# Performance work log

Measured on AMD Instinct MI355X. Metric: run time of the kernel, lower is better.

## Reference

```python
import jax, jax.numpy as jnp
import numpy as np

KERNEL_SIZE = 32
STRIDE = 16
NEG_INF = -1e30


def setup_inputs() -> dict:
    key = jax.random.key(0)
    ks = jax.random.split(key, 5)
    B, N, QH, KH, D = 1, 8192, 32, 2, 128
    q = jax.random.normal(ks[0], (B, N, QH, D), jnp.float32)
    k = jax.random.normal(ks[1], (B, N, KH, D), jnp.float32)
    v = jax.random.normal(ks[2], (B, N, KH, D), jnp.float32)
    weight = jax.random.uniform(ks[3], (KERNEL_SIZE,), jnp.float32)
    pe = jax.random.normal(ks[4], (KERNEL_SIZE, D), jnp.float32) * 0.02
    return {"q": q, "k": k, "v": v, "weight": weight, "pe": pe}


def block_compress(x, weight, pe, stride, kernel_size):
    # x: [B,N,H,D], weight: [K], pe: [K,D] -> y: [B,M,H,D]
    B, N, H, D = x.shape
    M = (N - kernel_size) // stride + 1
    idx = jnp.arange(M)[:, None] * stride + jnp.arange(kernel_size)[None, :]  # [M,K]
    xb = x[:, idx]  # [B,M,K,H,D] strided gather of overlapping blocks
    w_sum = jnp.maximum(jnp.sum(weight), 1e-6)
    y = jnp.einsum('bmkhd,k->bmhd', xb + pe[None, :, None, :][None], weight) / w_sum
    return y


def reference(q, k, v, weight, pe):
    B, N, QH, D = q.shape
    KH = k.shape[2]
    G = QH // KH
    sm_scale = D ** -0.5

    ck = block_compress(k, weight, pe, STRIDE, KERNEL_SIZE)  # [B,M,KH,D]
    cv = block_compress(v, weight, pe, STRIDE, KERNEL_SIZE)  # [B,M,KH,D]
    M = ck.shape[1]

    qg = q.reshape(B, N, KH, G, D)
    # scores: [B,KH,G,N,M]
    scores = jnp.einsum('bnkgd,bmkd->bkgnm', qg, ck) * sm_scale

    # causal block mask: query i sees compressed block j iff block fully in past
    i = jnp.arange(N)[:, None]
    j = jnp.arange(M)[None, :]
    mask = (j * STRIDE + KERNEL_SIZE) <= (i + 1)  # [N,M]
    valid_any = mask.any(axis=-1)  # [N]

    scores = jnp.where(mask[None, None, None], scores, NEG_INF)
    p = jax.nn.softmax(scores, axis=-1)
    p = jnp.where(valid_any[None, None, None, :, None], p, 0.0)

    out = jnp.einsum('bkgnm,bmkd->bnkgd', p, cv).reshape(B, N, QH, D)
    return out
```

## Files before the change

### kernel.cpp

```cpp
#include <hip/hip_runtime.h>
#include <hip/hip_bf16.h>

typedef __attribute__((ext_vector_type(8))) short short8;
typedef __attribute__((ext_vector_type(4))) float f32x4;

#define NSEQ 8192
#define NQH 32
#define NKH 2
#define NG 16
#define ND 128
#define NM 511
#define MPAD 512
#define SM_SCALE 0.08838834764831845f

__device__ __forceinline__ unsigned short f2bf(float f) {
  unsigned int u = __builtin_bit_cast(unsigned int, f);
  u += 0x7fffu + ((u >> 16) & 1u);
  return (unsigned short)(u >> 16);
}

__global__ __launch_bounds__(128)
void nsa_compress(const float* __restrict__ kin, const float* __restrict__ vin,
                  const float* __restrict__ weight, const float* __restrict__ pe,
                  unsigned short* __restrict__ ck, unsigned short* __restrict__ cvT)
{
  const int h = (int)blockIdx.x >> 9;
  const int m = (int)blockIdx.x & (MPAD - 1);
  const int d = (int)threadIdx.x;
  if (m >= NM) {
    ck[((size_t)h*MPAD + m)*ND + d] = 0;
    cvT[((size_t)h*ND + d)*MPAD + m] = 0;
    return;
  }
  float wsum = 0.f;
  #pragma unroll
  for (int j = 0; j < 32; ++j) wsum += weight[j];
  wsum = fmaxf(wsum, 1e-6f);
  const float inv = 1.0f / wsum;
  float ak = 0.f, av = 0.f;
  const int base = (m*16)*NKH*ND + h*ND + d;
  #pragma unroll
  for (int j = 0; j < 32; ++j) {
    const float w = weight[j];
    const float p = pe[j*ND + d];
    ak += w * (kin[base + j*NKH*ND] + p);
    av += w * (vin[base + j*NKH*ND] + p);
  }
  ck[((size_t)h*MPAD + m)*ND + d]  = f2bf(ak * inv);
  cvT[((size_t)h*ND + d)*MPAD + m] = f2bf(av * inv);
}

__global__ __launch_bounds__(256)
void nsa_attn(const float* __restrict__ q,
              const unsigned short* __restrict__ ck,
              const unsigned short* __restrict__ cvT,
              float* __restrict__ out)
{
  __shared__ short p_lds[2][4][2][16][32];
  const int tid = (int)threadIdx.x;
  const int w   = tid >> 6;
  const int l   = tid & 63;
  const int lq  = l >> 4;
  const int lm  = l & 15;

  const int h  = (int)blockIdx.x & 1;
  const int ib = (int)blockIdx.x >> 1;
  const int i0 = ib*8 + (w >> 1)*4;
  const int gb = (w & 1)*8;

  short8 qa[2][4];
  {
    const int ia = i0 + (lm >> 2);
    #pragma unroll
    for (int t = 0; t < 2; ++t) {
      const int qh = h*NG + gb + t*4 + (l & 3);
      const float* qp = q + ((size_t)ia*NQH + qh)*ND;
      #pragma unroll
      for (int kc = 0; kc < 4; ++kc) {
        const float4 f0 = *(const float4*)(qp + kc*32 + lq*8);
        const float4 f1 = *(const float4*)(qp + kc*32 + lq*8 + 4);
        short8 a;
        a[0] = (short)f2bf(f0.x); a[1] = (short)f2bf(f0.y);
        a[2] = (short)f2bf(f0.z); a[3] = (short)f2bf(f0.w);
        a[4] = (short)f2bf(f1.x); a[5] = (short)f2bf(f1.y);
        a[6] = (short)f2bf(f1.z); a[7] = (short)f2bf(f1.w);
        qa[t][kc] = a;
      }
    }
  }

  const int i_row = i0 + lq;
  const int mmax  = (i_row >= 31) ? ((i_row - 31) >> 4) : -1;
  const int mlimw = ((i0 + 3) >= 31) ? ((i0 + 3 - 31) >> 4) : -1;
  const int nt    = (mlimw >= 0) ? ((mlimw + 32) >> 5) : 0;

  f32x4 accO[2][8];
  #pragma unroll
  for (int t = 0; t < 2; ++t)
    #pragma unroll
    for (int dt = 0; dt < 8; ++dt) accO[t][dt] = (f32x4){0.f, 0.f, 0.f, 0.f};
  float mx[2][4], sm[2][4];
  #pragma unroll
  for (int t = 0; t < 2; ++t)
    #pragma unroll
    for (int r = 0; r < 4; ++r) { mx[t][r] = -1e30f; sm[t][r] = 0.f; }

  const unsigned short* ckh = ck  + (size_t)h*MPAD*ND;
  const unsigned short* cvh = cvT + (size_t)h*ND*MPAD;

  for (int mt = 0; mt < nt; ++mt) {
    const int m0 = mt*32;
    f32x4 accS[2][2];
    #pragma unroll
    for (int t = 0; t < 2; ++t)
      #pragma unroll
      for (int c = 0; c < 2; ++c) accS[t][c] = (f32x4){0.f, 0.f, 0.f, 0.f};
    #pragma unroll
    for (int kc = 0; kc < 4; ++kc) {
      const short8 b0 = *(const short8*)(ckh + (size_t)(m0 + lm)*ND      + kc*32 + lq*8);
      const short8 b1 = *(const short8*)(ckh + (size_t)(m0 + 16 + lm)*ND + kc*32 + lq*8);
      #pragma unroll
      for (int t = 0; t < 2; ++t) {
        accS[t][0] = __builtin_amdgcn_mfma_f32_16x16x32_bf16(qa[t][kc], b0, accS[t][0], 0, 0, 0);
        accS[t][1] = __builtin_amdgcn_mfma_f32_16x16x32_bf16(qa[t][kc], b1, accS[t][1], 0, 0, 0);
      }
    }
    #pragma unroll
    for (int t = 0; t < 2; ++t) {
      float pm0[4], pm1[4];
      #pragma unroll
      for (int r = 0; r < 4; ++r) {
        const float s0 = accS[t][0][r]*SM_SCALE;
        const float s1 = accS[t][1][r]*SM_SCALE;
        pm0[r] = ((m0 + lm)      <= mmax) ? s0 : -1e30f;
        pm1[r] = ((m0 + 16 + lm) <= mmax) ? s1 : -1e30f;
      }
      #pragma unroll
      for (int r = 0; r < 4; ++r) {
        float t0 = fmaxf(pm0[r], pm1[r]);
        t0 = fmaxf(t0, __shfl_xor(t0, 1));
        t0 = fmaxf(t0, __shfl_xor(t0, 2));
        t0 = fmaxf(t0, __shfl_xor(t0, 4));
        t0 = fmaxf(t0, __shfl_xor(t0, 8));
        const float mnew = fmaxf(mx[t][r], t0);
        const float resc = __expf(mx[t][r] - mnew);
        mx[t][r] = mnew;
        const float p0 = __expf(pm0[r] - mnew);
        const float p1 = __expf(pm1[r] - mnew);
        float rs = p0 + p1;
        rs += __shfl_xor(rs, 1);
        rs += __shfl_xor(rs, 2);
        rs += __shfl_xor(rs, 4);
        rs += __shfl_xor(rs, 8);
        sm[t][r] = sm[t][r]*resc + rs;
        #pragma unroll
        for (int dt = 0; dt < 8; ++dt) accO[t][dt][r] *= resc;
        p_lds[mt & 1][w][t][lq*4 + r][lm]      = (short)f2bf(p0);
        p_lds[mt & 1][w][t][lq*4 + r][16 + lm] = (short)f2bf(p1);
      }
    }
    asm volatile("s_waitcnt lgkmcnt(0)" ::: "memory");
    short8 pa[2];
    #pragma unroll
    for (int t = 0; t < 2; ++t)
      pa[t] = *(const short8*)(&p_lds[mt & 1][w][t][lm][lq*8]);
    #pragma unroll
    for (int dt = 0; dt < 8; ++dt) {
      const short8 bv = *(const short8*)(cvh + (size_t)(dt*16 + lm)*MPAD + m0 + lq*8);
      #pragma unroll
      for (int t = 0; t < 2; ++t)
        accO[t][dt] = __builtin_amdgcn_mfma_f32_16x16x32_bf16(pa[t], bv, accO[t][dt], 0, 0, 0);
    }
  }

  #pragma unroll
  for (int t = 0; t < 2; ++t) {
    #pragma unroll
    for (int r = 0; r < 4; ++r) {
      const float rinv = (mmax >= 0) ? (1.0f / sm[t][r]) : 0.0f;
      const int qh = h*NG + gb + t*4 + r;
      float* op = out + ((size_t)i_row*NQH + qh)*ND;
      #pragma unroll
      for (int dt = 0; dt < 8; ++dt)
        op[dt*16 + lm] = accO[t][dt][r] * rinv;
    }
  }
}

extern "C" void kernel_launch(void* const* d_in, const int* in_sizes, int n_in,
                              void* d_out, int out_size, void* d_ws, size_t ws_size,
                              hipStream_t stream)
{
  const float* q  = (const float*)d_in[0];
  const float* k  = (const float*)d_in[1];
  const float* v  = (const float*)d_in[2];
  const float* wt = (const float*)d_in[3];
  const float* pe = (const float*)d_in[4];
  float* outp = (float*)d_out;
  unsigned short* ck  = (unsigned short*)d_ws;
  unsigned short* cvT = ck + (size_t)NKH*MPAD*ND;
  nsa_compress<<<NKH*MPAD, 128, 0, stream>>>(k, v, wt, pe, ck, cvT);
  nsa_attn<<<2048, 256, 0, stream>>>(q, ck, cvT, outp);
}
```

Baseline: 431.9 us.

## Rewrite attention with 32x32 MFMA, register-resident P, lazy rescale and staged stores

The attention kernel moves from 16x16x32 to 32x32x16 bf16 MFMAs and computes S transposed, so each wave handles 32 query rows, which are 2 positions times 16 grouped heads. The P matrix now stays in registers, packed with v_cvt_pk and a lane swap, so it no longer goes through LDS. The online softmax only rescales when the running max grows by more than a threshold. Q is staged through swizzled LDS with the softmax scale folded in, blocks are issued in reverse order so the longest rows start first, and the output is transposed in LDS so it can be written with coalesced float4 stores. The compress kernel now does 4 compressed positions per block, factors out the pe term, and writes cvT with vector stores. The deferred rescale lets values grow up to e^8 before renormalizing, which is a small numerical risk.

```diff
diff --git a/kernel.cpp b/kernel.cpp
--- a/kernel.cpp
+++ b/kernel.cpp
@@ -3,6 +3,7 @@
 
 typedef __attribute__((ext_vector_type(8))) short short8;
 typedef __attribute__((ext_vector_type(4))) float f32x4;
+typedef __attribute__((ext_vector_type(16))) float f32x16;
 
 #define NSEQ 8192
 #define NQH 32
@@ -12,6 +13,7 @@
 #define NM 511
 #define MPAD 512
 #define SM_SCALE 0.08838834764831845f
+#define DEFER_THR 8.0f
 
 __device__ __forceinline__ unsigned short f2bf(float f) {
   unsigned int u = __builtin_bit_cast(unsigned int, f);
@@ -19,171 +21,216 @@
   return (unsigned short)(u >> 16);
 }
 
+__device__ __forceinline__ int cvtpk(float lo, float hi) {
+  int r; asm("v_cvt_pk_bf16_f32 %0, %1, %2" : "=v"(r) : "v"(lo), "v"(hi)); return r;
+}
+
+__device__ __forceinline__ float swap_max(float x) {
+  return fmaxf(x, __shfl_xor(x, 32));
+}
+
+__device__ __forceinline__ float swap_add(float x) {
+  return x + __shfl_xor(x, 32);
+}
+
 __global__ __launch_bounds__(128)
 void nsa_compress(const float* __restrict__ kin, const float* __restrict__ vin,
-                  const float* __restrict__ weight, const float* __restrict__ pe,
+                  const float* __restrict__ wt, const float* __restrict__ pe,
                   unsigned short* __restrict__ ck, unsigned short* __restrict__ cvT)
 {
-  const int h = (int)blockIdx.x >> 9;
-  const int m = (int)blockIdx.x & (MPAD - 1);
-  const int d = (int)threadIdx.x;
-  if (m >= NM) {
-    ck[((size_t)h*MPAD + m)*ND + d] = 0;
-    cvT[((size_t)h*ND + d)*MPAD + m] = 0;
-    return;
-  }
-  float wsum = 0.f;
-  #pragma unroll
-  for (int j = 0; j < 32; ++j) wsum += weight[j];
-  wsum = fmaxf(wsum, 1e-6f);
-  const float inv = 1.0f / wsum;
-  float ak = 0.f, av = 0.f;
-  const int base = (m*16)*NKH*ND + h*ND + d;
-  #pragma unroll
-  for (int j = 0; j < 32; ++j) {
-    const float w = weight[j];
-    const float p = pe[j*ND + d];
-    ak += w * (kin[base + j*NKH*ND] + p);
-    av += w * (vin[base + j*NKH*ND] + p);
-  }
-  ck[((size_t)h*MPAD + m)*ND + d]  = f2bf(ak * inv);
-  cvT[((size_t)h*ND + d)*MPAD + m] = f2bf(av * inv);
-}
-
-__global__ __launch_bounds__(256)
+  const int h  = (int)blockIdx.x >> 7;
+  const int m0 = ((int)blockIdx.x & 127) * 4;
+  const int d  = (int)threadIdx.x;
+
+  float w[32]; float wsum = 0.f;
+  #pragma unroll
+  for (int j = 0; j < 32; ++j) { w[j] = wt[j]; wsum += w[j]; }
+  const float inv = 1.0f / fmaxf(wsum, 1e-6f);
+  float pb = 0.f;
+  #pragma unroll
+  for (int j = 0; j < 32; ++j) pb += w[j] * pe[j*ND + d];
+
+  unsigned short rk[4], rv[4];
+  #pragma unroll
+  for (int mm = 0; mm < 4; ++mm) {
+    const int m = m0 + mm;
+    float sk = 0.f, sv = 0.f;
+    if (m < NM) {
+      const int rb = m * 16;
+      #pragma unroll
+      for (int j = 0; j < 32; ++j) {
+        const size_t off = ((size_t)(rb + j)*NKH + h)*ND + d;
+        sk += w[j] * kin[off];
+        sv += w[j] * vin[off];
+      }
+      rk[mm] = f2bf((sk + pb) * inv);
+      rv[mm] = f2bf((sv + pb) * inv);
+    } else { rk[mm] = 0; rv[mm] = 0; }
+    ck[((size_t)h*MPAD + m)*ND + d] = rk[mm];
+  }
+  ushort4 pv; pv.x = rv[0]; pv.y = rv[1]; pv.z = rv[2]; pv.w = rv[3];
+  *(ushort4*)(cvT + ((size_t)h*ND + d)*MPAD + m0) = pv;
+}
+
+__global__ __launch_bounds__(256, 2)
 void nsa_attn(const float* __restrict__ q,
               const unsigned short* __restrict__ ck,
               const unsigned short* __restrict__ cvT,
               float* __restrict__ out)
 {
-  __shared__ short p_lds[2][4][2][16][32];
+  __shared__ __align__(16) char smem[32768];
   const int tid = (int)threadIdx.x;
-  const int w   = tid >> 6;
-  const int l   = tid & 63;
-  const int lq  = l >> 4;
-  const int lm  = l & 15;
-
-  const int h  = (int)blockIdx.x & 1;
-  const int ib = (int)blockIdx.x >> 1;
-  const int i0 = ib*8 + (w >> 1)*4;
-  const int gb = (w & 1)*8;
-
-  short8 qa[2][4];
+  const int w = tid >> 6, l = tid & 63;
+  const int lo5 = l & 31, hi = l >> 5;
+  const int h = (int)blockIdx.x & 1;
+  const int ib = 1023 - ((int)blockIdx.x >> 1);
+  const int i_base = ib * 8;
+
   {
-    const int ia = i0 + (lm >> 2);
-    #pragma unroll
-    for (int t = 0; t < 2; ++t) {
-      const int qh = h*NG + gb + t*4 + (l & 3);
-      const float* qp = q + ((size_t)ia*NQH + qh)*ND;
-      #pragma unroll
-      for (int kc = 0; kc < 4; ++kc) {
-        const float4 f0 = *(const float4*)(qp + kc*32 + lq*8);
-        const float4 f1 = *(const float4*)(qp + kc*32 + lq*8 + 4);
-        short8 a;
-        a[0] = (short)f2bf(f0.x); a[1] = (short)f2bf(f0.y);
-        a[2] = (short)f2bf(f0.z); a[3] = (short)f2bf(f0.w);
-        a[4] = (short)f2bf(f1.x); a[5] = (short)f2bf(f1.y);
-        a[6] = (short)f2bf(f1.z); a[7] = (short)f2bf(f1.w);
-        qa[t][kc] = a;
-      }
-    }
-  }
-
-  const int i_row = i0 + lq;
-  const int mmax  = (i_row >= 31) ? ((i_row - 31) >> 4) : -1;
-  const int mlimw = ((i0 + 3) >= 31) ? ((i0 + 3 - 31) >> 4) : -1;
-  const int nt    = (mlimw >= 0) ? ((mlimw + 32) >> 5) : 0;
-
-  f32x4 accO[2][8];
-  #pragma unroll
-  for (int t = 0; t < 2; ++t)
-    #pragma unroll
-    for (int dt = 0; dt < 8; ++dt) accO[t][dt] = (f32x4){0.f, 0.f, 0.f, 0.f};
-  float mx[2][4], sm[2][4];
-  #pragma unroll
-  for (int t = 0; t < 2; ++t)
-    #pragma unroll
-    for (int r = 0; r < 4; ++r) { mx[t][r] = -1e30f; sm[t][r] = 0.f; }
+    const int r = tid >> 1, half = tid & 1;
+    const float* qp = q + ((size_t)(i_base + (r >> 4))*NQH + h*NG + (r & 15))*ND + half*64;
+    char* base = smem + r*256;
+    #pragma unroll
+    for (int jj = 0; jj < 8; ++jj) {
+      const float4 f0 = *(const float4*)(qp + jj*8);
+      const float4 f1 = *(const float4*)(qp + jj*8 + 4);
+      short8 a;
+      a[0] = (short)f2bf(f0.x*SM_SCALE); a[1] = (short)f2bf(f0.y*SM_SCALE);
+      a[2] = (short)f2bf(f0.z*SM_SCALE); a[3] = (short)f2bf(f0.w*SM_SCALE);
+      a[4] = (short)f2bf(f1.x*SM_SCALE); a[5] = (short)f2bf(f1.y*SM_SCALE);
+      a[6] = (short)f2bf(f1.z*SM_SCALE); a[7] = (short)f2bf(f1.w*SM_SCALE);
+      *(short8*)(base + ((half*128 + jj*16) ^ ((r & 7) << 4))) = a;
+    }
+  }
+  __syncthreads();
+
+  short8 qf[8];
+  {
+    const int r = w*32 + lo5;
+    const char* base = smem + r*256;
+    #pragma unroll
+    for (int kc = 0; kc < 8; ++kc)
+      qf[kc] = *(const short8*)(base + ((kc*32 + hi*16) ^ ((r & 7) << 4)));
+  }
+
+  const int ilo    = i_base + 2*w;
+  const int i_lane = ilo + (lo5 >> 4);
+  const int mmax    = (i_lane >= 31) ? ((i_lane - 31) >> 4) : -1;
+  const int mmax_lo = (ilo    >= 31) ? ((ilo    - 31) >> 4) : -1;
+  const int mlim    = (ilo + 1 >= 31) ? ((ilo + 1 - 31) >> 4) : -1;
+  const int nt      = (mlim >= 0) ? ((mlim + 32) >> 5) : 0;
+
+  f32x16 o[4];
+  #pragma unroll
+  for (int dt = 0; dt < 4; ++dt)
+    #pragma unroll
+    for (int rg = 0; rg < 16; ++rg) o[dt][rg] = 0.f;
+  float mx = -1e30f, sml = 0.f;
 
   const unsigned short* ckh = ck  + (size_t)h*MPAD*ND;
   const unsigned short* cvh = cvT + (size_t)h*ND*MPAD;
+  const unsigned short* kbase = ckh + (size_t)lo5*ND + hi*8;
+  const unsigned short* vbase = cvh + (size_t)lo5*MPAD + hi*8;
 
   for (int mt = 0; mt < nt; ++mt) {
-    const int m0 = mt*32;
-    f32x4 accS[2][2];
-    #pragma unroll
-    for (int t = 0; t < 2; ++t)
+    const int m0 = mt * 32;
+
+    short8 kf[8];
+    const unsigned short* kp = kbase + (size_t)m0*ND;
+    #pragma unroll
+    for (int kc = 0; kc < 8; ++kc) kf[kc] = *(const short8*)(kp + kc*16);
+    f32x16 s;
+    #pragma unroll
+    for (int rg = 0; rg < 16; ++rg) s[rg] = 0.f;
+    #pragma unroll
+    for (int kc = 0; kc < 8; ++kc)
+      s = __builtin_amdgcn_mfma_f32_32x32x16_bf16(kf[kc], qf[kc], s, 0, 0, 0);
+
+    float sv[16];
+    #pragma unroll
+    for (int rg = 0; rg < 16; ++rg) sv[rg] = s[rg];
+    if (m0 + 31 > mmax_lo) {
       #pragma unroll
-      for (int c = 0; c < 2; ++c) accS[t][c] = (f32x4){0.f, 0.f, 0.f, 0.f};
-    #pragma unroll
-    for (int kc = 0; kc < 4; ++kc) {
-      const short8 b0 = *(const short8*)(ckh + (size_t)(m0 + lm)*ND      + kc*32 + lq*8);
-      const short8 b1 = *(const short8*)(ckh + (size_t)(m0 + 16 + lm)*ND + kc*32 + lq*8);
+      for (int rg = 0; rg < 16; ++rg) {
+        const int mr = m0 + (rg & 3) + 8*(rg >> 2) + 4*hi;
+        sv[rg] = (mr <= mmax) ? sv[rg] : -1e30f;
+      }
+    }
+
+    float t0 = fmaxf(sv[0], sv[1]),   t1 = fmaxf(sv[2], sv[3]);
+    float t2 = fmaxf(sv[4], sv[5]),   t3 = fmaxf(sv[6], sv[7]);
+    float t4 = fmaxf(sv[8], sv[9]),   t5 = fmaxf(sv[10], sv[11]);
+    float t6 = fmaxf(sv[12], sv[13]), t7 = fmaxf(sv[14], sv[15]);
+    t0 = fmaxf(t0, t1); t2 = fmaxf(t2, t3); t4 = fmaxf(t4, t5); t6 = fmaxf(t6, t7);
+    float cand = swap_max(fmaxf(fmaxf(t0, t2), fmaxf(t4, t6)));
+    if (__any(cand > mx + DEFER_THR)) {
+      const float nmx = fmaxf(mx, cand);
+      const float resc = __expf(mx - nmx);
+      mx = nmx;
+      sml *= resc;
       #pragma unroll
-      for (int t = 0; t < 2; ++t) {
-        accS[t][0] = __builtin_amdgcn_mfma_f32_16x16x32_bf16(qa[t][kc], b0, accS[t][0], 0, 0, 0);
-        accS[t][1] = __builtin_amdgcn_mfma_f32_16x16x32_bf16(qa[t][kc], b1, accS[t][1], 0, 0, 0);
-      }
-    }
-    #pragma unroll
-    for (int t = 0; t < 2; ++t) {
-      float pm0[4], pm1[4];
-      #pragma unroll
-      for (int r = 0; r < 4; ++r) {
-        const float s0 = accS[t][0][r]*SM_SCALE;
-        const float s1 = accS[t][1][r]*SM_SCALE;
-        pm0[r] = ((m0 + lm)      <= mmax) ? s0 : -1e30f;
-        pm1[r] = ((m0 + 16 + lm) <= mmax) ? s1 : -1e30f;
-      }
-      #pragma unroll
-      for (int r = 0; r < 4; ++r) {
-        float t0 = fmaxf(pm0[r], pm1[r]);
-        t0 = fmaxf(t0, __shfl_xor(t0, 1));
-        t0 = fmaxf(t0, __shfl_xor(t0, 2));
-        t0 = fmaxf(t0, __shfl_xor(t0, 4));
-        t0 = fmaxf(t0, __shfl_xor(t0, 8));
-        const float mnew = fmaxf(mx[t][r], t0);
-        const float resc = __expf(mx[t][r] - mnew);
-        mx[t][r] = mnew;
-        const float p0 = __expf(pm0[r] - mnew);
-        const float p1 = __expf(pm1[r] - mnew);
-        float rs = p0 + p1;
-        rs += __shfl_xor(rs, 1);
-        rs += __shfl_xor(rs, 2);
-        rs += __shfl_xor(rs, 4);
-        rs += __shfl_xor(rs, 8);
-        sm[t][r] = sm[t][r]*resc + rs;
+      for (int dt = 0; dt < 4; ++dt)
         #pragma unroll
-        for (int dt = 0; dt < 8; ++dt) accO[t][dt][r] *= resc;
-        p_lds[mt & 1][w][t][lq*4 + r][lm]      = (short)f2bf(p0);
-        p_lds[mt & 1][w][t][lq*4 + r][16 + lm] = (short)f2bf(p1);
-      }
+        for (int rg = 0; rg < 16; ++rg) o[dt][rg] *= resc;
+    }
+
+    float p[16];
+    #pragma unroll
+    for (int rg = 0; rg < 16; ++rg) p[rg] = __expf(sv[rg] - mx);
+    float s0 = (p[0]+p[1]) + (p[2]+p[3]),   s1 = (p[4]+p[5]) + (p[6]+p[7]);
+    float s2 = (p[8]+p[9]) + (p[10]+p[11]), s3 = (p[12]+p[13]) + (p[14]+p[15]);
+    sml += (s0 + s1) + (s2 + s3);
+
+    int d0 = cvtpk(p[0], p[1]),   d1 = cvtpk(p[2], p[3]);
+    int d2 = cvtpk(p[4], p[5]),   d3 = cvtpk(p[6], p[7]);
+    int d4 = cvtpk(p[8], p[9]),   d5 = cvtpk(p[10], p[11]);
+    int d6 = cvtpk(p[12], p[13]), d7 = cvtpk(p[14], p[15]);
+    const int x0 = __shfl_xor(d0, 32), x1 = __shfl_xor(d1, 32);
+    const int x2 = __shfl_xor(d2, 32), x3 = __shfl_xor(d3, 32);
+    const int x4 = __shfl_xor(d4, 32), x5 = __shfl_xor(d5, 32);
+    const int x6 = __shfl_xor(d6, 32), x7 = __shfl_xor(d7, 32);
+    const bool hib = (hi != 0);
+    int4 pf0i = { hib ? x2 : d0, hib ? x3 : d1, hib ? d2 : x0, hib ? d3 : x1 };
+    int4 pf1i = { hib ? x6 : d4, hib ? x7 : d5, hib ? d6 : x4, hib ? d7 : x5 };
+    const short8 pf0 = __builtin_bit_cast(short8, pf0i);
+    const short8 pf1 = __builtin_bit_cast(short8, pf1i);
+
+    #pragma unroll
+    for (int dt = 0; dt < 4; ++dt) {
+      const unsigned short* vp = vbase + (size_t)dt*32*MPAD + m0;
+      const short8 vf0 = *(const short8*)(vp);
+      const short8 vf1 = *(const short8*)(vp + 16);
+      o[dt] = __builtin_amdgcn_mfma_f32_32x32x16_bf16(vf0, pf0, o[dt], 0, 0, 0);
+      o[dt] = __builtin_amdgcn_mfma_f32_32x32x16_bf16(vf1, pf1, o[dt], 0, 0, 0);
+    }
+  }
+
+  const float sfull = swap_add(sml);
+  const float rinv = (mmax >= 0 && sfull > 0.f) ? 1.0f / sfull : 0.f;
+
+  float* T = (float*)(smem + w*8192);
+  const int q2 = l >> 1, xh = l & 1;
+  float* op = out + ((size_t)(i_base + 2*w + (q2 >> 4))*NQH + h*NG + (q2 & 15))*ND;
+  #pragma unroll
+  for (int dt = 0; dt < 4; ++dt) {
+    #pragma unroll
+    for (int rg = 0; rg < 16; ++rg) {
+      const int dp = (rg & 3) + 8*(rg >> 2) + 4*hi;
+      T[lo5*33 + dp] = o[dt][rg] * rinv;
     }
     asm volatile("s_waitcnt lgkmcnt(0)" ::: "memory");
-    short8 pa[2];
-    #pragma unroll
-    for (int t = 0; t < 2; ++t)
-      pa[t] = *(const short8*)(&p_lds[mt & 1][w][t][lm][lq*8]);
-    #pragma unroll
-    for (int dt = 0; dt < 8; ++dt) {
-      const short8 bv = *(const short8*)(cvh + (size_t)(dt*16 + lm)*MPAD + m0 + lq*8);
-      #pragma unroll
-      for (int t = 0; t < 2; ++t)
-        accO[t][dt] = __builtin_amdgcn_mfma_f32_16x16x32_bf16(pa[t], bv, accO[t][dt], 0, 0, 0);
-    }
-  }
-
-  #pragma unroll
-  for (int t = 0; t < 2; ++t) {
-    #pragma unroll
-    for (int r = 0; r < 4; ++r) {
-      const float rinv = (mmax >= 0) ? (1.0f / sm[t][r]) : 0.0f;
-      const int qh = h*NG + gb + t*4 + r;
-      float* op = out + ((size_t)i_row*NQH + qh)*ND;
-      #pragma unroll
-      for (int dt = 0; dt < 8; ++dt)
-        op[dt*16 + lm] = accO[t][dt][r] * rinv;
-    }
+    __builtin_amdgcn_sched_barrier(0);
+    #pragma unroll
+    for (int cc = 0; cc < 4; ++cc) {
+      float4 vv;
+      vv.x = T[q2*33 + xh*16 + cc*4 + 0];
+      vv.y = T[q2*33 + xh*16 + cc*4 + 1];
+      vv.z = T[q2*33 + xh*16 + cc*4 + 2];
+      vv.w = T[q2*33 + xh*16 + cc*4 + 3];
+      *(float4*)(op + dt*32 + xh*16 + cc*4) = vv;
+    }
+    asm volatile("s_waitcnt lgkmcnt(0)" ::: "memory");
+    __builtin_amdgcn_sched_barrier(0);
   }
 }
 
@@ -199,6 +246,6 @@
   float* outp = (float*)d_out;
   unsigned short* ck  = (unsigned short*)d_ws;
   unsigned short* cvT = ck + (size_t)NKH*MPAD*ND;
-  nsa_compress<<<NKH*MPAD, 128, 0, stream>>>(k, v, wt, pe, ck, cvT);
+  nsa_compress<<<256, 128, 0, stream>>>(k, v, wt, pe, ck, cvT);
   nsa_attn<<<2048, 256, 0, stream>>>(q, ck, cvT, outp);
 }
```

Result: faster. 396.3 us (-8.3%).
